# Kernel optimization log

Hardware: AMD Instinct MI355X
Metric: run time of the kernel (lower is better)

## Reference

```python
import jax, jax.numpy as jnp
from jax import lax
import numpy as np

B, T, D, H, OUT = 2048, 512, 1, 50, 3


def setup_inputs() -> dict:
    key = jax.random.key(0)
    ks = jax.random.split(key, 7)
    s = 1.0 / np.sqrt(H)  # PyTorch LSTM init scale
    x = jax.random.normal(ks[0], (B, T, D), dtype=jnp.float32)
    W_ih = jax.random.uniform(ks[1], (4 * H, D), minval=-s, maxval=s, dtype=jnp.float32)
    W_hh = jax.random.uniform(ks[2], (4 * H, H), minval=-s, maxval=s, dtype=jnp.float32)
    b_ih = jax.random.uniform(ks[3], (4 * H,), minval=-s, maxval=s, dtype=jnp.float32)
    b_hh = jax.random.uniform(ks[4], (4 * H,), minval=-s, maxval=s, dtype=jnp.float32)
    fc_w = jax.random.uniform(ks[5], (OUT, H), minval=-s, maxval=s, dtype=jnp.float32)
    fc_b = jax.random.uniform(ks[6], (OUT,), minval=-s, maxval=s, dtype=jnp.float32)
    return {"x": x, "W_ih": W_ih, "W_hh": W_hh, "b_ih": b_ih, "b_hh": b_hh,
            "fc_w": fc_w, "fc_b": fc_b}


def reference(x, W_ih, W_hh, b_ih, b_hh, fc_w, fc_b):
    # x: [B, T, 1]; PyTorch gate order: i, f, g, o
    b = x.shape[0]
    h = H
    # Precompute input projection for all timesteps: [B, T, 4H]
    x_proj = jnp.einsum('btd,gd->btg', x, W_ih) + b_ih + b_hh

    def step(carry, xp_t):
        h_t, c_t = carry
        gates = xp_t + h_t @ W_hh.T  # [B, 4H]
        i = jax.nn.sigmoid(gates[:, 0 * h:1 * h])
        f = jax.nn.sigmoid(gates[:, 1 * h:2 * h])
        g = jnp.tanh(gates[:, 2 * h:3 * h])
        o = jax.nn.sigmoid(gates[:, 3 * h:4 * h])
        c_new = f * c_t + i * g
        h_new = o * jnp.tanh(c_new)
        return (h_new, c_new), None

    h0 = jnp.zeros((b, h), dtype=x.dtype)
    c0 = jnp.zeros((b, h), dtype=x.dtype)
    (h_T, _), _ = lax.scan(step, (h0, c0), jnp.swapaxes(x_proj, 0, 1))
    # fc on last timestep hidden state only (out[:, -1, :])
    return h_T @ fc_w.T + fc_b
```

## Files before the change

### kernel.cpp

```cpp
#include <hip/hip_runtime.h>


#define BB 2048
#define TT 512
#define HH 50
#define NB 16
#define NW 16
#define XP 513
#define HS 72
#define XSC   32.0f
#define XSCI  0.03125f
#define L1 -1.4426950408889634f
#define L2 -2.8853900817779268f

typedef __attribute__((ext_vector_type(4))) float          f32x4;
typedef __attribute__((ext_vector_type(8))) _Float16       f16x8;
typedef __attribute__((ext_vector_type(4))) unsigned short u16x4;

__global__ __launch_bounds__(NW * 64)
void lstm_r16_kernel(const float* __restrict__ x,
                     const float* __restrict__ W_ih,
                     const float* __restrict__ W_hh,
                     const float* __restrict__ b_ih,
                     const float* __restrict__ b_hh,
                     const float* __restrict__ fc_w,
                     const float* __restrict__ fc_b,
                     float* __restrict__ out) {
    __shared__ float xs[NB * XP];
    __shared__ __align__(16) unsigned short hf[2][NB][HS];
    __shared__ float hfin[NB][64];

    const int tid  = threadIdx.x;
    const int w    = tid >> 6;
    const int lane = tid & 63;
    const int hi   = lane >> 4;
    const int bcol = lane & 15;
    const int b0   = blockIdx.x * NB;

    for (int idx = tid; idx < NB * TT; idx += NW * 64) {
        xs[(idx >> 9) * XP + (idx & 511)] = x[(b0 + (idx >> 9)) * TT + (idx & 511)];
    }
    if (tid < NB) xs[tid * XP + 512] = 0.0f;
    for (int idx = tid; idx < (int)(sizeof(hf) / 4); idx += NW * 64) {
        ((unsigned*)hf)[idx] = 0;
    }

    const int ga = bcol & 3;
    const int ua = 4 * w + (bcol >> 2);
    const bool ok = (ua < HH);
    const float Lg = (ga == 2) ? L2 : L1;
    f16x8 Ah0, Ah1;
    #pragma unroll
    for (int s = 0; s < 2; ++s) {
        #pragma unroll
        for (int e = 0; e < 8; ++e) {
            const int k = 32 * s + 8 * hi + e;
            _Float16 ah = (_Float16)0.0f;
            if (ok) {
                if (k < HH) {
                    ah = (_Float16)(Lg * W_hh[(ga * HH + ua) * HH + k]);
                } else if (k == 61) {
                    ah = (_Float16)(Lg * W_ih[ga * HH + ua] * XSCI);
                } else if (k == 63) {
                    ah = (_Float16)(Lg * W_ih[ga * HH + ua]);
                }
            }
            if (s == 0) Ah0[e] = ah; else Ah1[e] = ah;
        }
    }

    f32x4 bias_c;
    #pragma unroll
    for (int r = 0; r < 4; ++r) {
        const int u = 4 * w + hi;
        const float Lr = (r == 2) ? L2 : L1;
        bias_c[r] = (u < HH) ? Lr * (b_ih[r * HH + u] + b_hh[r * HH + u]) : 0.0f;
    }

    const unsigned short* rb  = &hf[0][bcol][8 * hi];
    unsigned short*       wb  = &hf[0][bcol][4 * w + hi];
    unsigned short*       xwb = &hf[0][bcol][0];
    const bool xwriter = (w == 15) && (hi == 3);
    const bool hwriter = (4 * w + hi) < HH;

    __syncthreads();

    if (xwriter) {
        const float x0 = xs[bcol * XP + 0];
        const _Float16 xh = (_Float16)x0;
        const _Float16 xl = (_Float16)((x0 - (float)xh) * XSC);
        u16x4 P = {0, __builtin_bit_cast(unsigned short, xl), 0,
                      __builtin_bit_cast(unsigned short, xh)};
        *(u16x4*)(xwb + 60) = P;
    }

    float c = 0.0f, hcur = 0.0f;

    __syncthreads();

#define STEP(CB, T) { \
        const f16x8 B0 = *(const f16x8*)(rb + (CB) * 1152); \
        const f16x8 B1 = *(const f16x8*)(rb + (CB) * 1152 + 32); \
        f32x4 acc = __builtin_amdgcn_mfma_f32_16x16x32_f16(Ah0, B0, bias_c, 0, 0, 0); \
        acc = __builtin_amdgcn_mfma_f32_16x16x32_f16(Ah1, B1, acc, 0, 0, 0); \
        const float E1 = __builtin_amdgcn_exp2f(acc[0]);    \
        const float E2 = __builtin_amdgcn_exp2f(acc[1]);    \
        const float G  = __builtin_amdgcn_exp2f(acc[2]);    \
        const float E4 = __builtin_amdgcn_exp2f(acc[3]);    \
        const float P1 = 1.0f + E1, P2 = 1.0f + E2; \
        const float PG = 1.0f + G,  P4 = 1.0f + E4; \
        const float MG = 1.0f - G; \
        const float N  = fmaf(c * P1, PG, MG * P2); \
        const float D  = (P1 * P2) * PG; \
        c = N * __builtin_amdgcn_rcpf(D); \
        const float C5 = __builtin_amdgcn_exp2f(L2 * c); \
        const float Q  = (1.0f + C5) * P4; \
        hcur = (1.0f - C5) * __builtin_amdgcn_rcpf(Q); \
        if (hwriter) \
            wb[(1 - (CB)) * 1152] = __builtin_bit_cast(unsigned short, (_Float16)hcur); \
        if (xwriter) { \
            const float xn = xs[bcol * XP + (T) + 1]; \
            const _Float16 xh = (_Float16)xn; \
            const _Float16 xl = (_Float16)((xn - (float)xh) * XSC); \
            u16x4 P = {0, __builtin_bit_cast(unsigned short, xl), 0, \
                          __builtin_bit_cast(unsigned short, xh)}; \
            *(u16x4*)(xwb + (1 - (CB)) * 1152 + 60) = P; \
        } \
        __syncthreads(); }

    #pragma unroll 1
    for (int t = 0; t < TT; t += 2) {
        STEP(0, t)
        STEP(1, t + 1)
    }
#undef STEP

    hfin[bcol][4 * w + hi] = hcur;
    __syncthreads();
    if (tid < NB * 3) {
        const int b = tid / 3, o = tid % 3;
        float s = fc_b[o];
        for (int uu = 0; uu < HH; ++uu)
            s = fmaf(hfin[b][uu], fc_w[o * HH + uu], s);
        out[(b0 + b) * 3 + o] = s;
    }
}

extern "C" void kernel_launch(void* const* d_in, const int* in_sizes, int n_in,
                              void* d_out, int out_size, void* d_ws, size_t ws_size,
                              hipStream_t stream) {
    const float* x    = (const float*)d_in[0];
    const float* W_ih = (const float*)d_in[1];
    const float* W_hh = (const float*)d_in[2];
    const float* b_ih = (const float*)d_in[3];
    const float* b_hh = (const float*)d_in[4];
    const float* fc_w = (const float*)d_in[5];
    const float* fc_b = (const float*)d_in[6];
    float* out = (float*)d_out;

    dim3 grid(BB / NB);
    dim3 block(NW * 64);
    lstm_r16_kernel<<<grid, block, 0, stream>>>(x, W_ih, W_hh, b_ih, b_hh,
                                                fc_w, fc_b, out);
}
```

Before: 262.0 us.

## Interleave two independent batch groups per block to overlap MFMA and gate math

Each block now handles two groups of 16 batch rows, A and B, and alternates between them. The matrix multiply for one group is issued while the elementwise gate update for the other group runs, which hides the dependent latency of the serial recurrence. The grid shrinks to 64 blocks. The x staging in shared memory is replaced by per-step global loads prefetched one step ahead. This halves the number of blocks, which can leave many CUs idle on a large GPU, and adds a global load to the critical loop.

```diff
diff --git a/kernel.cpp b/kernel.cpp
--- a/kernel.cpp
+++ b/kernel.cpp
@@ -6,7 +6,6 @@
 #define HH 50
 #define NB 16
 #define NW 16
-#define XP 513
 #define HS 72
 #define XSC   32.0f
 #define XSCI  0.03125f
@@ -17,8 +16,10 @@
 typedef __attribute__((ext_vector_type(8))) _Float16       f16x8;
 typedef __attribute__((ext_vector_type(4))) unsigned short u16x4;
 
+#define F16BITS(v) __builtin_bit_cast(unsigned short, (_Float16)(v))
+
 __global__ __launch_bounds__(NW * 64)
-void lstm_r16_kernel(const float* __restrict__ x,
+void lstm_r17_kernel(const float* __restrict__ x,
                      const float* __restrict__ W_ih,
                      const float* __restrict__ W_hh,
                      const float* __restrict__ b_ih,
@@ -26,23 +27,20 @@
                      const float* __restrict__ fc_w,
                      const float* __restrict__ fc_b,
                      float* __restrict__ out) {
-    __shared__ float xs[NB * XP];
-    __shared__ __align__(16) unsigned short hf[2][NB][HS];
-    __shared__ float hfin[NB][64];
+    __shared__ __align__(16) unsigned short hfA[2][NB][HS];
+    __shared__ __align__(16) unsigned short hfB[2][NB][HS];
+    __shared__ float hfin[2][NB][64];
 
     const int tid  = threadIdx.x;
     const int w    = tid >> 6;
     const int lane = tid & 63;
     const int hi   = lane >> 4;
     const int bcol = lane & 15;
-    const int b0   = blockIdx.x * NB;
+    const int b0   = blockIdx.x * (2 * NB);
 
-    for (int idx = tid; idx < NB * TT; idx += NW * 64) {
-        xs[(idx >> 9) * XP + (idx & 511)] = x[(b0 + (idx >> 9)) * TT + (idx & 511)];
-    }
-    if (tid < NB) xs[tid * XP + 512] = 0.0f;
-    for (int idx = tid; idx < (int)(sizeof(hf) / 4); idx += NW * 64) {
-        ((unsigned*)hf)[idx] = 0;
+    for (int idx = tid; idx < (int)(sizeof(hfA) / 4); idx += NW * 64) {
+        ((unsigned*)hfA)[idx] = 0;
+        ((unsigned*)hfB)[idx] = 0;
     }
 
     const int ga = bcol & 3;
@@ -77,72 +75,107 @@
         bias_c[r] = (u < HH) ? Lr * (b_ih[r * HH + u] + b_hh[r * HH + u]) : 0.0f;
     }
 
-    const unsigned short* rb  = &hf[0][bcol][8 * hi];
-    unsigned short*       wb  = &hf[0][bcol][4 * w + hi];
-    unsigned short*       xwb = &hf[0][bcol][0];
+    const unsigned short* rbA = &hfA[0][bcol][8 * hi];
+    const unsigned short* rbB = &hfB[0][bcol][8 * hi];
+    unsigned short* wbA  = &hfA[0][bcol][4 * w + hi];
+    unsigned short* wbB  = &hfB[0][bcol][4 * w + hi];
+    unsigned short* xwbA = &hfA[0][bcol][0];
+    unsigned short* xwbB = &hfB[0][bcol][0];
     const bool xwriter = (w == 15) && (hi == 3);
     const bool hwriter = (4 * w + hi) < HH;
+
+#define AUGW(PTR, XV) { \
+        const _Float16 xh_ = (_Float16)(XV); \
+        const _Float16 xl_ = (_Float16)(((XV) - (float)xh_) * XSC); \
+        u16x4 P_ = {0, __builtin_bit_cast(unsigned short, xl_), 0, \
+                       __builtin_bit_cast(unsigned short, xh_)}; \
+        *(u16x4*)((PTR) + 60) = P_; }
+
+    float xAn = 0.0f, xBn = 0.0f;
 
     __syncthreads();
 
     if (xwriter) {
-        const float x0 = xs[bcol * XP + 0];
-        const _Float16 xh = (_Float16)x0;
-        const _Float16 xl = (_Float16)((x0 - (float)xh) * XSC);
-        u16x4 P = {0, __builtin_bit_cast(unsigned short, xl), 0,
-                      __builtin_bit_cast(unsigned short, xh)};
-        *(u16x4*)(xwb + 60) = P;
+        const float xa0 = x[(b0 + bcol) * TT + 0];
+        const float xb0 = x[(b0 + NB + bcol) * TT + 0];
+        AUGW(xwbA, xa0)
+        AUGW(xwbB, xb0)
+        xAn = x[(b0 + bcol) * TT + 1];
+        xBn = x[(b0 + NB + bcol) * TT + 1];
     }
 
-    float c = 0.0f, hcur = 0.0f;
+    float cA = 0.0f, cB = 0.0f, hA = 0.0f, hB = 0.0f;
+    f32x4 accA, accB;
 
     __syncthreads();
 
-#define STEP(CB, T) { \
-        const f16x8 B0 = *(const f16x8*)(rb + (CB) * 1152); \
-        const f16x8 B1 = *(const f16x8*)(rb + (CB) * 1152 + 32); \
-        f32x4 acc = __builtin_amdgcn_mfma_f32_16x16x32_f16(Ah0, B0, bias_c, 0, 0, 0); \
-        acc = __builtin_amdgcn_mfma_f32_16x16x32_f16(Ah1, B1, acc, 0, 0, 0); \
-        const float E1 = __builtin_amdgcn_exp2f(acc[0]);    \
-        const float E2 = __builtin_amdgcn_exp2f(acc[1]);    \
-        const float G  = __builtin_amdgcn_exp2f(acc[2]);    \
-        const float E4 = __builtin_amdgcn_exp2f(acc[3]);    \
+#define UPDATE(ACC, CC, HO) { \
+        const float E1 = __builtin_amdgcn_exp2f((ACC)[0]);    \
+        const float E2 = __builtin_amdgcn_exp2f((ACC)[1]);    \
+        const float G  = __builtin_amdgcn_exp2f((ACC)[2]);    \
+        const float E4 = __builtin_amdgcn_exp2f((ACC)[3]);    \
         const float P1 = 1.0f + E1, P2 = 1.0f + E2; \
         const float PG = 1.0f + G,  P4 = 1.0f + E4; \
         const float MG = 1.0f - G; \
-        const float N  = fmaf(c * P1, PG, MG * P2); \
+        const float N  = fmaf((CC) * P1, PG, MG * P2); \
         const float D  = (P1 * P2) * PG; \
-        c = N * __builtin_amdgcn_rcpf(D); \
-        const float C5 = __builtin_amdgcn_exp2f(L2 * c); \
+        CC = N * __builtin_amdgcn_rcpf(D); \
+        const float C5 = __builtin_amdgcn_exp2f(L2 * (CC)); \
         const float Q  = (1.0f + C5) * P4; \
-        hcur = (1.0f - C5) * __builtin_amdgcn_rcpf(Q); \
-        if (hwriter) \
-            wb[(1 - (CB)) * 1152] = __builtin_bit_cast(unsigned short, (_Float16)hcur); \
-        if (xwriter) { \
-            const float xn = xs[bcol * XP + (T) + 1]; \
-            const _Float16 xh = (_Float16)xn; \
-            const _Float16 xl = (_Float16)((xn - (float)xh) * XSC); \
-            u16x4 P = {0, __builtin_bit_cast(unsigned short, xl), 0, \
-                          __builtin_bit_cast(unsigned short, xh)}; \
-            *(u16x4*)(xwb + (1 - (CB)) * 1152 + 60) = P; \
-        } \
-        __syncthreads(); }
+        HO = (1.0f - C5) * __builtin_amdgcn_rcpf(Q); }
+
+    {
+        const f16x8 B0_ = *(const f16x8*)(rbA);
+        const f16x8 B1_ = *(const f16x8*)(rbA + 32);
+        accA = __builtin_amdgcn_mfma_f32_16x16x32_f16(Ah0, B0_, bias_c, 0, 0, 0);
+        accA = __builtin_amdgcn_mfma_f32_16x16x32_f16(Ah1, B1_, accA, 0, 0, 0);
+        __syncthreads();
+    }
 
     #pragma unroll 1
-    for (int t = 0; t < TT; t += 2) {
-        STEP(0, t)
-        STEP(1, t + 1)
+    for (int t = 0; t < TT; ++t) {
+        const int cb  = t & 1;
+        const int nb2 = 1 - cb;
+        {
+            const f16x8 B0_ = *(const f16x8*)(rbB + cb * 1152);
+            const f16x8 B1_ = *(const f16x8*)(rbB + cb * 1152 + 32);
+            UPDATE(accA, cA, hA)
+            if (hwriter) wbA[nb2 * 1152] = F16BITS(hA);
+            if (xwriter) {
+                AUGW(xwbA + nb2 * 1152, xAn)
+                xAn = x[(b0 + bcol) * TT + ((t + 2 < TT) ? (t + 2) : (TT - 1))];
+            }
+            accB = __builtin_amdgcn_mfma_f32_16x16x32_f16(Ah0, B0_, bias_c, 0, 0, 0);
+            accB = __builtin_amdgcn_mfma_f32_16x16x32_f16(Ah1, B1_, accB, 0, 0, 0);
+            __syncthreads();
+        }
+        {
+            const f16x8 B0_ = *(const f16x8*)(rbA + nb2 * 1152);
+            const f16x8 B1_ = *(const f16x8*)(rbA + nb2 * 1152 + 32);
+            UPDATE(accB, cB, hB)
+            if (hwriter) wbB[nb2 * 1152] = F16BITS(hB);
+            if (xwriter) {
+                AUGW(xwbB + nb2 * 1152, xBn)
+                xBn = x[(b0 + NB + bcol) * TT + ((t + 2 < TT) ? (t + 2) : (TT - 1))];
+            }
+            accA = __builtin_amdgcn_mfma_f32_16x16x32_f16(Ah0, B0_, bias_c, 0, 0, 0);
+            accA = __builtin_amdgcn_mfma_f32_16x16x32_f16(Ah1, B1_, accA, 0, 0, 0);
+            __syncthreads();
+        }
     }
-#undef STEP
+#undef UPDATE
+#undef AUGW
 
-    hfin[bcol][4 * w + hi] = hcur;
+    hfin[0][bcol][4 * w + hi] = hA;
+    hfin[1][bcol][4 * w + hi] = hB;
     __syncthreads();
-    if (tid < NB * 3) {
-        const int b = tid / 3, o = tid % 3;
+    if (tid < 2 * NB * 3) {
+        const int bl = tid / 3, o = tid % 3;
+        const int g = bl >> 4, bc = bl & 15;
         float s = fc_b[o];
         for (int uu = 0; uu < HH; ++uu)
-            s = fmaf(hfin[b][uu], fc_w[o * HH + uu], s);
-        out[(b0 + b) * 3 + o] = s;
+            s = fmaf(hfin[g][bc][uu], fc_w[o * HH + uu], s);
+        out[(b0 + bl) * 3 + o] = s;
     }
 }
 
@@ -158,8 +191,8 @@
     const float* fc_b = (const float*)d_in[6];
     float* out = (float*)d_out;
 
-    dim3 grid(BB / NB);
+    dim3 grid(BB / (2 * NB));
     dim3 block(NW * 64);
-    lstm_r16_kernel<<<grid, block, 0, stream>>>(x, W_ih, W_hh, b_ih, b_hh,
+    lstm_r17_kernel<<<grid, block, 0, stream>>>(x, W_ih, W_hh, b_ih, b_hh,
                                                 fc_w, fc_b, out);
 }
```

After: 460.2 us. +75.7%, slower.
